# Kernel optimization log

Measured on AMD Instinct MI355X. Metric: run time of the kernel, lower is better.

## Reference

```python
import jax, jax.numpy as jnp
import numpy as np
import math

B, S, D, H, N = 4, 2048, 1024, 8, 128  # batch, seq_len, d_model, n_heads, num_osc
ITERS = 10
DT = 0.1
PI = math.pi


def setup_inputs() -> dict:
    key = jax.random.key(0)
    ks = jax.random.split(key, 5)
    return {
        "x": jax.random.normal(ks[0], (B, S, D), jnp.float32),
        "mask": jnp.ones((B, S), jnp.int32),
        "W_phase": jax.random.normal(ks[1], (D, H * N), jnp.float32) / math.sqrt(D),
        "b_phase": jnp.zeros((H * N,), jnp.float32),
        "natural_freq": jax.random.normal(ks[2], (H, N), jnp.float32) * 0.1,
        "coupling": jnp.ones((H, 1, 1), jnp.float32),  # coupling_strength = 1.0
        "W_out": jax.random.normal(ks[3], (H * N, D), jnp.float32) / math.sqrt(H * N),
        "b_out": jnp.zeros((D,), jnp.float32),
    }


def reference(x, mask, W_phase, b_phase, natural_freq, coupling, W_out, b_out):
    # phases: [B, H, S, N]
    ph = (x @ W_phase + b_phase).reshape(B, S, H, N).transpose(0, 2, 1, 3)
    ph = jnp.tanh(ph) * PI
    m = mask.astype(ph.dtype)[:, None, :, None]  # [B,1,S,1] mask over j
    K = coupling.reshape(1, H, 1, 1)
    w = natural_freq.reshape(1, H, 1, N)

    def step(ph, _):
        s = jnp.sin(ph)
        c = jnp.cos(ph)
        # mean_j m_j * sin(theta_i - theta_j) = sin(th_i)*mean(m*cos) - cos(th_i)*mean(m*sin)
        ms = (m * s).mean(axis=2, keepdims=True)  # [B,H,1,N]
        mc = (m * c).mean(axis=2, keepdims=True)
        dtheta = w + K * (s * mc - c * ms)
        ph2 = jnp.mod(ph + DT * dtheta + PI, 2 * PI) - PI
        return ph2, None

    ph, _ = jax.lax.scan(step, ph, None, length=ITERS)
    # from_phase; dropout is identity in eval mode
    y = ph.transpose(0, 2, 1, 3).reshape(B, S, H * N) @ W_out + b_out
    return y
```

## Files before the change

### kernel.cpp

```cpp
#include <hip/hip_runtime.h>
#include <math.h>

#define S_ 2048
#define D_ 1024
#define HN_ 1024
#define B_ 4
#define M_ 8192
#define K1_ 3072
#define K3_ 1024
#define ITERS_ 10
#define DT_ 0.1f
#define PI_ 3.14159265358979323846f
#define TWOPI_ 6.28318530717958647692f
#define INV2PI_ 0.15915494309189533577f
#define SCALE_ 4096.0f
#define INVSC2_ (1.0f / 16777216.0f)

typedef __attribute__((ext_vector_type(8))) _Float16 f16x8;
typedef __attribute__((ext_vector_type(4))) float f32x4;

__device__ ushort g_xs [(size_t)M_ * K1_];
__device__ ushort g_WpT[(size_t)HN_ * K1_];
__device__ float  g_ph [(size_t)B_ * HN_ * S_];
__device__ ushort g_phh[(size_t)B_ * HN_ * S_];
__device__ ushort g_phT[(size_t)M_ * HN_];
__device__ ushort g_WoT[(size_t)D_ * HN_];

__device__ __forceinline__ ushort f2h(float f) {
    union { _Float16 h; ushort u; } v; v.h = (_Float16)f; return v.u;
}
__device__ __forceinline__ void split2s(float x, ushort& A, ushort& Bc) {
    const float xs = x * SCALE_;
    union { _Float16 h; ushort u; } va, vb;
    va.h = (_Float16)xs;
    const float r = xs - (float)va.h;
    vb.h = (_Float16)r;
    A = va.u; Bc = vb.u;
}
__device__ __forceinline__ void gload16(const void* g, void* l) {
    __builtin_amdgcn_global_load_lds(
        (const __attribute__((address_space(1))) void*)g,
        (__attribute__((address_space(3))) void*)l, 16, 0, 0);
}
__device__ __forceinline__ int pack2(ushort a, ushort b) {
    return (int)(unsigned)a | ((int)(unsigned)b << 16);
}

__global__ __launch_bounds__(256) void split_x(const float* __restrict__ X) {
    const int idx = blockIdx.x * 256 + threadIdx.x;
    const float4 v = ((const float4*)X)[idx];
    const int m  = idx >> 8;
    const int k4 = (idx & 255) * 4;
    ushort a[4], b[4];
    split2s(v.x, a[0], b[0]);
    split2s(v.y, a[1], b[1]);
    split2s(v.z, a[2], b[2]);
    split2s(v.w, a[3], b[3]);
    ushort* row = g_xs + (size_t)m * K1_ + k4;
    int2 oa; oa.x = pack2(a[0], a[1]); oa.y = pack2(a[2], a[3]);
    int2 ob; ob.x = pack2(b[0], b[1]); ob.y = pack2(b[2], b[3]);
    *(int2*)(row)        = oa;
    *(int2*)(row + 1024) = oa;
    *(int2*)(row + 2048) = ob;
}

__global__ __launch_bounds__(256) void splitT_Wp(const float* __restrict__ Wp) {
    __shared__ float t[64][68];
    const int k0 = blockIdx.x * 64;
    const int n0 = blockIdx.y * 64;
    const int r = threadIdx.x >> 2;
    const int c = (threadIdx.x & 3) * 16;
    const float* src = Wp + (size_t)(k0 + r) * HN_ + n0 + c;
    #pragma unroll
    for (int q = 0; q < 4; ++q)
        *(float4*)&t[r][c + 4 * q] = ((const float4*)src)[q];
    __syncthreads();
    ushort ha[16], hb[16];
    #pragma unroll
    for (int j = 0; j < 16; ++j)
        split2s(t[c + j][r], ha[j], hb[j]);
    int4 a0, a1, b0, b1;
    a0.x = pack2(ha[0], ha[1]);   a0.y = pack2(ha[2], ha[3]);
    a0.z = pack2(ha[4], ha[5]);   a0.w = pack2(ha[6], ha[7]);
    a1.x = pack2(ha[8], ha[9]);   a1.y = pack2(ha[10], ha[11]);
    a1.z = pack2(ha[12], ha[13]); a1.w = pack2(ha[14], ha[15]);
    b0.x = pack2(hb[0], hb[1]);   b0.y = pack2(hb[2], hb[3]);
    b0.z = pack2(hb[4], hb[5]);   b0.w = pack2(hb[6], hb[7]);
    b1.x = pack2(hb[8], hb[9]);   b1.y = pack2(hb[10], hb[11]);
    b1.z = pack2(hb[12], hb[13]); b1.w = pack2(hb[14], hb[15]);
    ushort* dst = g_WpT + (size_t)(n0 + r) * K1_ + k0 + c;
    *(int4*)(dst)            = a0; *(int4*)(dst + 8)        = a1;
    *(int4*)(dst + 1024)     = b0; *(int4*)(dst + 1032)     = b1;
    *(int4*)(dst + 2048)     = a0; *(int4*)(dst + 2056)     = a1;
}

__global__ __launch_bounds__(256) void castT_Wo(const float* __restrict__ Wo) {
    __shared__ float t[64][68];
    const int k0 = blockIdx.x * 64;
    const int n0 = blockIdx.y * 64;
    const int r = threadIdx.x >> 2;
    const int c = (threadIdx.x & 3) * 16;
    const float* src = Wo + (size_t)(k0 + r) * D_ + n0 + c;
    #pragma unroll
    for (int q = 0; q < 4; ++q)
        *(float4*)&t[r][c + 4 * q] = ((const float4*)src)[q];
    __syncthreads();
    ushort h[16];
    #pragma unroll
    for (int j = 0; j < 16; ++j) h[j] = f2h(t[c + j][r]);
    ushort* dst = g_WoT + (size_t)(n0 + r) * HN_ + k0 + c;
    int4 o0, o1;
    o0.x = pack2(h[0], h[1]);   o0.y = pack2(h[2], h[3]);
    o0.z = pack2(h[4], h[5]);   o0.w = pack2(h[6], h[7]);
    o1.x = pack2(h[8], h[9]);   o1.y = pack2(h[10], h[11]);
    o1.z = pack2(h[12], h[13]); o1.w = pack2(h[14], h[15]);
    *(int4*)dst = o0;
    *(int4*)(dst + 8) = o1;
}

template<int KDIM>
__device__ __forceinline__ void gemm_mainloop(const ushort* __restrict__ A,
                                              const ushort* __restrict__ Bm,
                                              ushort* lds,
                                              int m0, int n0, int wid, int l,
                                              int wm, int wn,
                                              f32x4 (&acc)[4][4]) {
    constexpr int NT = KDIM / 64;
    const int r8   = l >> 3;
    const int swzo = ((l & 7) * 16) ^ (r8 << 4);

    #define STAGE(T, BUF) do {                                                   \
        const size_t gb_ = (size_t)(T) * 128 + swzo;                             \
        char* ab_ = (char*)lds + (BUF) * 49152;                                  \
        _Pragma("unroll")                                                        \
        for (int j_ = 0; j_ < 4; ++j_) {                                         \
            const int c_ = wid * 4 + j_;                                         \
            gload16((const char*)(A + (size_t)(m0 + c_ * 8 + r8) * KDIM) + gb_,  \
                    ab_ + c_ * 1024);                                            \
        }                                                                        \
        _Pragma("unroll")                                                        \
        for (int j_ = 0; j_ < 2; ++j_) {                                         \
            const int c_ = wid * 2 + j_;                                         \
            gload16((const char*)(Bm + (size_t)(n0 + c_ * 8 + r8) * KDIM) + gb_, \
                    ab_ + 32768 + c_ * 1024);                                    \
        }                                                                        \
    } while (0)

    STAGE(0, 0);
    STAGE(1, 1);

    for (int t = 0; t < NT; ++t) {
        if (t < NT - 1) asm volatile("s_waitcnt vmcnt(6)" ::: "memory");
        else            asm volatile("s_waitcnt vmcnt(0)" ::: "memory");
        __builtin_amdgcn_sched_barrier(0);
        __builtin_amdgcn_s_barrier();
        __builtin_amdgcn_sched_barrier(0);
        if (t + 2 < NT) STAGE(t + 2, (t + 2) % 3);

        const char* ab = (const char*)lds + (t % 3) * 49152;
        const char* bb = ab + 32768;
        #pragma unroll
        for (int ks = 0; ks < 2; ++ks) {
            const int kb = ks * 64 + (l >> 4) * 16;
            f16x8 af[4], bf[4];
            #pragma unroll
            for (int i = 0; i < 4; ++i) {
                const int r = wm * 64 + i * 16 + (l & 15);
                af[i] = *(const f16x8*)(ab + r * 128 + (kb ^ ((r & 7) << 4)));
            }
            #pragma unroll
            for (int i = 0; i < 4; ++i) {
                const int r = wn * 64 + i * 16 + (l & 15);
                bf[i] = *(const f16x8*)(bb + r * 128 + (kb ^ ((r & 7) << 4)));
            }
            __builtin_amdgcn_s_setprio(1);
            #pragma unroll
            for (int i = 0; i < 4; ++i)
                #pragma unroll
                for (int jj = 0; jj < 4; ++jj)
                    acc[i][jj] = __builtin_amdgcn_mfma_f32_16x16x32_f16(af[i], bf[jj], acc[i][jj], 0, 0, 0);
            __builtin_amdgcn_s_setprio(0);
        }
    }
    #undef STAGE
}

__global__ __launch_bounds__(512) void gemm1(const float* __restrict__ bias) {
    __shared__ ushort lds[3 * 24576];
    const int tid = threadIdx.x;
    const int wid = tid >> 6, l = tid & 63;
    const int bid = blockIdx.x;
    const int swz = (bid & 7) * 32 + (bid >> 3);
    const int m0 = (swz & 31) * 256, n0 = (swz >> 5) * 128;
    const int wm = wid >> 1, wn = wid & 1;

    f32x4 acc[4][4];
    #pragma unroll
    for (int i = 0; i < 4; ++i)
        #pragma unroll
        for (int j = 0; j < 4; ++j) acc[i][j] = (f32x4){0.f, 0.f, 0.f, 0.f};

    gemm_mainloop<K1_>(g_xs, g_WpT, lds, m0, n0, wid, l, wm, wn, acc);

    const int r4 = (l >> 4) * 4;
    const int cn = l & 15;
    #pragma unroll
    for (int i = 0; i < 4; ++i) {
        const int mg = m0 + wm * 64 + i * 16 + r4;
        const int bidx = mg >> 11;
        const int sg = mg & 2047;
        #pragma unroll
        for (int jj = 0; jj < 4; ++jj) {
            const int ng = n0 + wn * 64 + jj * 16 + cn;
            const float bb = bias[ng];
            float4 o;
            o.x = PI_ * tanhf(fmaf(acc[i][jj][0], INVSC2_, bb));
            o.y = PI_ * tanhf(fmaf(acc[i][jj][1], INVSC2_, bb));
            o.z = PI_ * tanhf(fmaf(acc[i][jj][2], INVSC2_, bb));
            o.w = PI_ * tanhf(fmaf(acc[i][jj][3], INVSC2_, bb));
            *(float4*)(g_ph + ((size_t)bidx * HN_ + ng) * S_ + sg) = o;
        }
    }
}

__global__ __launch_bounds__(512) void gemm3(const float* __restrict__ bias,
                                             float* __restrict__ Y) {
    __shared__ ushort lds[3 * 24576];
    const int tid = threadIdx.x;
    const int wid = tid >> 6, l = tid & 63;
    const int bid = blockIdx.x;
    const int swz = (bid & 7) * 32 + (bid >> 3);
    const int m0 = (swz & 31) * 256, n0 = (swz >> 5) * 128;
    const int wm = wid >> 1, wn = wid & 1;

    f32x4 acc[4][4];
    #pragma unroll
    for (int i = 0; i < 4; ++i)
        #pragma unroll
        for (int j = 0; j < 4; ++j) acc[i][j] = (f32x4){0.f, 0.f, 0.f, 0.f};

    gemm_mainloop<K3_>(g_phT, g_WoT, lds, m0, n0, wid, l, wm, wn, acc);

    const int r4 = (l >> 4) * 4;
    const int cn = l & 15;
    #pragma unroll
    for (int i = 0; i < 4; ++i) {
        const int mg = m0 + wm * 64 + i * 16 + r4;
        #pragma unroll
        for (int jj = 0; jj < 4; ++jj) {
            const int ng = n0 + wn * 64 + jj * 16 + cn;
            const float bb = bias[ng];
            #pragma unroll
            for (int r = 0; r < 4; ++r)
                Y[(size_t)(mg + r) * D_ + ng] = acc[i][jj][r] + bb;
        }
    }
}

__global__ __launch_bounds__(256) void kuramoto(const int* __restrict__ mask,
                                                const float* __restrict__ natf,
                                                const float* __restrict__ coup) {
    const int wave = blockIdx.x * 4 + (threadIdx.x >> 6);
    const int lane = threadIdx.x & 63;
    const int b = wave >> 10;
    const int hn = wave & 1023;
    const int h = hn >> 7;

    const float wf = natf[hn];
    const float K = coup[h];

    const float* base = g_ph + ((size_t)b * HN_ + hn) * S_;

    float ph[32];
    #pragma unroll
    for (int i = 0; i < 8; ++i) {
        float4 v = *(const float4*)(base + i * 256 + lane * 4);
        ph[4 * i + 0] = v.x; ph[4 * i + 1] = v.y;
        ph[4 * i + 2] = v.z; ph[4 * i + 3] = v.w;
    }

    const int* mb = mask + b * S_;
    unsigned mbits = 0;
    #pragma unroll
    for (int i = 0; i < 8; ++i) {
        int4 mv = *(const int4*)(mb + i * 256 + lane * 4);
        mbits |= (mv.x != 0 ? 1u : 0u) << (4 * i + 0);
        mbits |= (mv.y != 0 ? 1u : 0u) << (4 * i + 1);
        mbits |= (mv.z != 0 ? 1u : 0u) << (4 * i + 2);
        mbits |= (mv.w != 0 ? 1u : 0u) << (4 * i + 3);
    }

    for (int it = 0; it < ITERS_; ++it) {
        float s[32], c[32];
        float ls = 0.f, lc = 0.f;
        #pragma unroll
        for (int i = 0; i < 32; ++i) {
            s[i] = __sinf(ph[i]);
            c[i] = __cosf(ph[i]);
            const float mf = (float)((mbits >> i) & 1u);
            ls = fmaf(mf, s[i], ls);
            lc = fmaf(mf, c[i], lc);
        }
        #pragma unroll
        for (int off = 32; off; off >>= 1) {
            ls += __shfl_xor(ls, off);
            lc += __shfl_xor(lc, off);
        }
        const float ms = ls * (1.f / 2048.f);
        const float mc = lc * (1.f / 2048.f);
        #pragma unroll
        for (int i = 0; i < 32; ++i) {
            const float dth = fmaf(K, fmaf(s[i], mc, -c[i] * ms), wf);
            float t = fmaf(DT_, dth, ph[i]) + PI_;
            t -= TWOPI_ * floorf(t * INV2PI_);
            ph[i] = t - PI_;
        }
    }

    ushort* ob = g_phh + ((size_t)b * HN_ + hn) * S_;
    #pragma unroll
    for (int i = 0; i < 8; ++i) {
        ushort4 o;
        o.x = f2h(ph[4 * i + 0]); o.y = f2h(ph[4 * i + 1]);
        o.z = f2h(ph[4 * i + 2]); o.w = f2h(ph[4 * i + 3]);
        *(ushort4*)(ob + i * 256 + lane * 4) = o;
    }
}

__global__ __launch_bounds__(256) void transpose_ph() {
    __shared__ ushort t[64][72];
    const int b = blockIdx.z;
    const int h0 = blockIdx.y * 64;
    const int s0 = blockIdx.x * 64;
    const int r = threadIdx.x >> 2;
    const int c = (threadIdx.x & 3) * 16;
    const ushort* src = g_phh + ((size_t)b * HN_ + h0 + r) * S_ + s0 + c;
    *(int4*)&t[r][c] = *(const int4*)src;
    *(int4*)&t[r][c + 8] = *(const int4*)(src + 8);
    __syncthreads();
    ushort o[16];
    #pragma unroll
    for (int j = 0; j < 16; ++j) o[j] = t[c + j][r];
    ushort* dst = g_phT + ((size_t)(b * S_ + s0 + r)) * HN_ + h0 + c;
    int4 o0, o1;
    o0.x = pack2(o[0], o[1]);   o0.y = pack2(o[2], o[3]);
    o0.z = pack2(o[4], o[5]);   o0.w = pack2(o[6], o[7]);
    o1.x = pack2(o[8], o[9]);   o1.y = pack2(o[10], o[11]);
    o1.z = pack2(o[12], o[13]); o1.w = pack2(o[14], o[15]);
    *(int4*)dst = o0;
    *(int4*)(dst + 8) = o1;
}

extern "C" void kernel_launch(void* const* d_in, const int* in_sizes, int n_in,
                              void* d_out, int out_size, void* d_ws, size_t ws_size,
                              hipStream_t stream) {
    const float* x    = (const float*)d_in[0];
    const int*   mask = (const int*)d_in[1];
    const float* Wp   = (const float*)d_in[2];
    const float* bp   = (const float*)d_in[3];
    const float* natf = (const float*)d_in[4];
    const float* coup = (const float*)d_in[5];
    const float* Wo   = (const float*)d_in[6];
    const float* bo   = (const float*)d_in[7];
    float* y = (float*)d_out;

    split_x  <<<dim3(8192),         256, 0, stream>>>(x);
    splitT_Wp<<<dim3(16, 16),       256, 0, stream>>>(Wp);
    castT_Wo <<<dim3(16, 16),       256, 0, stream>>>(Wo);
    gemm1    <<<dim3(256),          512, 0, stream>>>(bp);
    kuramoto <<<dim3(1024),         256, 0, stream>>>(mask, natf, coup);
    transpose_ph<<<dim3(32, 16, 4), 256, 0, stream>>>();
    gemm3    <<<dim3(256),          512, 0, stream>>>(bo, y);
}
```

Measured before the change: 174.0 us.

## Split GEMM K-step into two phases interleaving loads with MFMA and remap tiles per XCD

Each 128-wide K tile in the shared GEMM mainloop is now split into two 64-wide halves. Each half reads its LDS fragments, issues half of the next global-to-LDS prefetch (A operand first, then B), barriers, and then runs its MFMAs under raised priority. The aim is to overlap global prefetch issue with matrix math and give finer-grained scheduling. Separately, the block-to-tile mapping is changed so that each XCD gets a contiguous 4x8 patch of output tiles, which should improve L2 reuse of the A and B operands. The trade-off is extra barriers per iteration, and the prefetches now complete on a different schedule relative to the vmcnt(6) wait.

```diff
diff --git a/kernel.cpp b/kernel.cpp
--- a/kernel.cpp
+++ b/kernel.cpp
@@ -129,7 +129,7 @@
     const int r8   = l >> 3;
     const int swzo = ((l & 7) * 16) ^ (r8 << 4);
 
-    #define STAGE(T, BUF) do {                                                   \
+    #define STAGE_A(T, BUF) do {                                                 \
         const size_t gb_ = (size_t)(T) * 128 + swzo;                             \
         char* ab_ = (char*)lds + (BUF) * 49152;                                  \
         _Pragma("unroll")                                                        \
@@ -138,16 +138,20 @@
             gload16((const char*)(A + (size_t)(m0 + c_ * 8 + r8) * KDIM) + gb_,  \
                     ab_ + c_ * 1024);                                            \
         }                                                                        \
+    } while (0)
+    #define STAGE_B(T, BUF) do {                                                 \
+        const size_t gb_ = (size_t)(T) * 128 + swzo;                             \
+        char* bb_ = (char*)lds + (BUF) * 49152 + 32768;                          \
         _Pragma("unroll")                                                        \
         for (int j_ = 0; j_ < 2; ++j_) {                                         \
             const int c_ = wid * 2 + j_;                                         \
             gload16((const char*)(Bm + (size_t)(n0 + c_ * 8 + r8) * KDIM) + gb_, \
-                    ab_ + 32768 + c_ * 1024);                                    \
+                    bb_ + c_ * 1024);                                            \
         }                                                                        \
     } while (0)
 
-    STAGE(0, 0);
-    STAGE(1, 1);
+    STAGE_A(0, 0); STAGE_B(0, 0);
+    STAGE_A(1, 1); STAGE_B(1, 1);
 
     for (int t = 0; t < NT; ++t) {
         if (t < NT - 1) asm volatile("s_waitcnt vmcnt(6)" ::: "memory");
@@ -155,14 +159,14 @@
         __builtin_amdgcn_sched_barrier(0);
         __builtin_amdgcn_s_barrier();
         __builtin_amdgcn_sched_barrier(0);
-        if (t + 2 < NT) STAGE(t + 2, (t + 2) % 3);
 
         const char* ab = (const char*)lds + (t % 3) * 49152;
         const char* bb = ab + 32768;
-        #pragma unroll
-        for (int ks = 0; ks < 2; ++ks) {
-            const int kb = ks * 64 + (l >> 4) * 16;
-            f16x8 af[4], bf[4];
+
+        f16x8 af[4], bf[4];
+
+        {
+            const int kb = (l >> 4) * 16;
             #pragma unroll
             for (int i = 0; i < 4; ++i) {
                 const int r = wm * 64 + i * 16 + (l & 15);
@@ -173,25 +177,65 @@
                 const int r = wn * 64 + i * 16 + (l & 15);
                 bf[i] = *(const f16x8*)(bb + r * 128 + (kb ^ ((r & 7) << 4)));
             }
-            __builtin_amdgcn_s_setprio(1);
-            #pragma unroll
-            for (int i = 0; i < 4; ++i)
-                #pragma unroll
-                for (int jj = 0; jj < 4; ++jj)
-                    acc[i][jj] = __builtin_amdgcn_mfma_f32_16x16x32_f16(af[i], bf[jj], acc[i][jj], 0, 0, 0);
-            __builtin_amdgcn_s_setprio(0);
-        }
-    }
-    #undef STAGE
+        }
+        if (t + 2 < NT) STAGE_A(t + 2, (t + 2) % 3);
+        __builtin_amdgcn_sched_barrier(0);
+        __builtin_amdgcn_s_barrier();
+        asm volatile("s_waitcnt lgkmcnt(0)" ::: "memory");
+        __builtin_amdgcn_sched_barrier(0);
+        __builtin_amdgcn_s_setprio(1);
+        #pragma unroll
+        for (int i = 0; i < 4; ++i)
+            #pragma unroll
+            for (int jj = 0; jj < 4; ++jj)
+                acc[i][jj] = __builtin_amdgcn_mfma_f32_16x16x32_f16(af[i], bf[jj], acc[i][jj], 0, 0, 0);
+        __builtin_amdgcn_s_setprio(0);
+        __builtin_amdgcn_sched_barrier(0);
+
+        {
+            const int kb = 64 + (l >> 4) * 16;
+            #pragma unroll
+            for (int i = 0; i < 4; ++i) {
+                const int r = wm * 64 + i * 16 + (l & 15);
+                af[i] = *(const f16x8*)(ab + r * 128 + (kb ^ ((r & 7) << 4)));
+            }
+            #pragma unroll
+            for (int i = 0; i < 4; ++i) {
+                const int r = wn * 64 + i * 16 + (l & 15);
+                bf[i] = *(const f16x8*)(bb + r * 128 + (kb ^ ((r & 7) << 4)));
+            }
+        }
+        if (t + 2 < NT) STAGE_B(t + 2, (t + 2) % 3);
+        __builtin_amdgcn_sched_barrier(0);
+        __builtin_amdgcn_s_barrier();
+        asm volatile("s_waitcnt lgkmcnt(0)" ::: "memory");
+        __builtin_amdgcn_sched_barrier(0);
+        __builtin_amdgcn_s_setprio(1);
+        #pragma unroll
+        for (int i = 0; i < 4; ++i)
+            #pragma unroll
+            for (int jj = 0; jj < 4; ++jj)
+                acc[i][jj] = __builtin_amdgcn_mfma_f32_16x16x32_f16(af[i], bf[jj], acc[i][jj], 0, 0, 0);
+        __builtin_amdgcn_s_setprio(0);
+        __builtin_amdgcn_sched_barrier(0);
+    }
+    #undef STAGE_A
+    #undef STAGE_B
+}
+
+__device__ __forceinline__ void tile_map(int bid, int& m0, int& n0) {
+    const int xcd = bid & 7;
+    const int idx = bid >> 3;
+    m0 = (xcd * 4 + (idx >> 3)) * 256;
+    n0 = (idx & 7) * 128;
 }
 
 __global__ __launch_bounds__(512) void gemm1(const float* __restrict__ bias) {
     __shared__ ushort lds[3 * 24576];
     const int tid = threadIdx.x;
     const int wid = tid >> 6, l = tid & 63;
-    const int bid = blockIdx.x;
-    const int swz = (bid & 7) * 32 + (bid >> 3);
-    const int m0 = (swz & 31) * 256, n0 = (swz >> 5) * 128;
+    int m0, n0;
+    tile_map(blockIdx.x, m0, n0);
     const int wm = wid >> 1, wn = wid & 1;
 
     f32x4 acc[4][4];
@@ -228,9 +272,8 @@
     __shared__ ushort lds[3 * 24576];
     const int tid = threadIdx.x;
     const int wid = tid >> 6, l = tid & 63;
-    const int bid = blockIdx.x;
-    const int swz = (bid & 7) * 32 + (bid >> 3);
-    const int m0 = (swz & 31) * 256, n0 = (swz >> 5) * 128;
+    int m0, n0;
+    tile_map(blockIdx.x, m0, n0);
     const int wm = wid >> 1, wn = wid & 1;
 
     f32x4 acc[4][4];
```

New measurement: 158.7 us. -8.8%, faster.

## Restructure GEMM mainloop into four interleaved phases with 128x256 tiles

Applied to the files above, without the earlier changes.

Changes the GEMM block tile from 256x128 to 128x256 with a 2x4 wave layout and a new XCD-aware tile mapping. The k-step is split into four phases, each interleaving LDS fragment loads, one slice of the next global stage and a quarter of the MFMAs, separated by barriers. Launch bounds now request two blocks per CU. The aim is to overlap global/LDS traffic with MFMA work and improve L2 locality, at the cost of extra barriers per k-step and more register pressure.

```diff
diff --git a/kernel.cpp b/kernel.cpp
--- a/kernel.cpp
+++ b/kernel.cpp
@@ -128,71 +128,135 @@
     constexpr int NT = KDIM / 64;
     const int r8   = l >> 3;
     const int swzo = ((l & 7) * 16) ^ (r8 << 4);
-
-    #define STAGE(T, BUF) do {                                                   \
-        const size_t gb_ = (size_t)(T) * 128 + swzo;                             \
-        char* ab_ = (char*)lds + (BUF) * 49152;                                  \
-        _Pragma("unroll")                                                        \
-        for (int j_ = 0; j_ < 4; ++j_) {                                         \
-            const int c_ = wid * 4 + j_;                                         \
-            gload16((const char*)(A + (size_t)(m0 + c_ * 8 + r8) * KDIM) + gb_,  \
-                    ab_ + c_ * 1024);                                            \
-        }                                                                        \
-        _Pragma("unroll")                                                        \
-        for (int j_ = 0; j_ < 2; ++j_) {                                         \
-            const int c_ = wid * 2 + j_;                                         \
-            gload16((const char*)(Bm + (size_t)(n0 + c_ * 8 + r8) * KDIM) + gb_, \
-                    ab_ + 32768 + c_ * 1024);                                    \
-        }                                                                        \
-    } while (0)
-
-    STAGE(0, 0);
-    STAGE(1, 1);
-
-    for (int t = 0; t < NT; ++t) {
-        if (t < NT - 1) asm volatile("s_waitcnt vmcnt(6)" ::: "memory");
-        else            asm volatile("s_waitcnt vmcnt(0)" ::: "memory");
-        __builtin_amdgcn_sched_barrier(0);
-        __builtin_amdgcn_s_barrier();
-        __builtin_amdgcn_sched_barrier(0);
-        if (t + 2 < NT) STAGE(t + 2, (t + 2) % 3);
-
-        const char* ab = (const char*)lds + (t % 3) * 49152;
-        const char* bb = ab + 32768;
-        #pragma unroll
-        for (int ks = 0; ks < 2; ++ks) {
-            const int kb = ks * 64 + (l >> 4) * 16;
-            f16x8 af[4], bf[4];
-            #pragma unroll
-            for (int i = 0; i < 4; ++i) {
-                const int r = wm * 64 + i * 16 + (l & 15);
-                af[i] = *(const f16x8*)(ab + r * 128 + (kb ^ ((r & 7) << 4)));
-            }
-            #pragma unroll
-            for (int i = 0; i < 4; ++i) {
-                const int r = wn * 64 + i * 16 + (l & 15);
-                bf[i] = *(const f16x8*)(bb + r * 128 + (kb ^ ((r & 7) << 4)));
-            }
-            __builtin_amdgcn_s_setprio(1);
-            #pragma unroll
-            for (int i = 0; i < 4; ++i)
-                #pragma unroll
-                for (int jj = 0; jj < 4; ++jj)
-                    acc[i][jj] = __builtin_amdgcn_mfma_f32_16x16x32_f16(af[i], bf[jj], acc[i][jj], 0, 0, 0);
-            __builtin_amdgcn_s_setprio(0);
-        }
-    }
-    #undef STAGE
-}
-
-__global__ __launch_bounds__(512) void gemm1(const float* __restrict__ bias) {
+    const int l15  = l & 15;
+    const int kq16 = (l >> 4) * 16;
+
+    #define STG_A(GB, BUF, H)                                                     \
+        gload16((const char*)(A + (size_t)(m0 + (H)*64 + wid*8 + r8) * KDIM) + (GB), \
+                (char*)lds + (BUF)*49152 + ((H)*64 + wid*8)*128)
+    #define STG_B(GB, BUF, H) do {                                                \
+        _Pragma("unroll")                                                         \
+        for (int j_ = 0; j_ < 2; ++j_)                                            \
+            gload16((const char*)(Bm + (size_t)(n0 + (H)*128 + (wid*2+j_)*8 + r8) * KDIM) + (GB), \
+                    (char*)lds + (BUF)*49152 + 16384 + ((H)*128 + (wid*2+j_)*8)*128); \
+    } while (0)
+    #define STG_KT(T, BUF) do {                                                   \
+        const size_t gb_ = (size_t)(T) * 128 + swzo;                              \
+        STG_A(gb_, BUF, 0); STG_A(gb_, BUF, 1);                                   \
+        STG_B(gb_, BUF, 0); STG_B(gb_, BUF, 1);                                   \
+    } while (0)
+
+    #define LD_A(MIB) do {                                                        \
+        _Pragma("unroll")                                                         \
+        for (int mi_ = 0; mi_ < 2; ++mi_)                                         \
+            _Pragma("unroll")                                                     \
+            for (int ks_ = 0; ks_ < 2; ++ks_) {                                   \
+                const int r_ = wm*64 + ((MIB)+mi_)*16 + l15;                      \
+                Aa[mi_][ks_] = *(const f16x8*)(ab + r_*128 +                      \
+                    ((ks_*64 + kq16) ^ ((r_ & 7) << 4)));                         \
+            }                                                                     \
+    } while (0)
+    #define LD_B(NIB) do {                                                        \
+        _Pragma("unroll")                                                         \
+        for (int ni_ = 0; ni_ < 2; ++ni_)                                         \
+            _Pragma("unroll")                                                     \
+            for (int ks_ = 0; ks_ < 2; ++ks_) {                                   \
+                const int r_ = wn*64 + ((NIB)+ni_)*16 + l15;                      \
+                Bb[(NIB)+ni_][ks_] = *(const f16x8*)(bb + r_*128 +                \
+                    ((ks_*64 + kq16) ^ ((r_ & 7) << 4)));                         \
+            }                                                                     \
+    } while (0)
+
+    #define PH_BAR_LGKM do {                                                      \
+        __builtin_amdgcn_sched_barrier(0);                                        \
+        __builtin_amdgcn_s_barrier();                                             \
+        asm volatile("s_waitcnt lgkmcnt(0)" ::: "memory");                        \
+        __builtin_amdgcn_sched_barrier(0);                                        \
+    } while (0)
+    #define PH_BAR do {                                                           \
+        __builtin_amdgcn_sched_barrier(0);                                        \
+        __builtin_amdgcn_s_barrier();                                             \
+        __builtin_amdgcn_sched_barrier(0);                                        \
+    } while (0)
+
+    #define PH_MFMA(MIB, NIB) do {                                                \
+        __builtin_amdgcn_s_setprio(1);                                            \
+        _Pragma("unroll")                                                         \
+        for (int mi_ = 0; mi_ < 2; ++mi_)                                         \
+            _Pragma("unroll")                                                     \
+            for (int ni_ = 0; ni_ < 2; ++ni_)                                     \
+                _Pragma("unroll")                                                 \
+                for (int ks_ = 0; ks_ < 2; ++ks_)                                 \
+                    acc[(MIB)+mi_][(NIB)+ni_] =                                   \
+                        __builtin_amdgcn_mfma_f32_16x16x32_f16(                   \
+                            Aa[mi_][ks_], Bb[(NIB)+ni_][ks_],                     \
+                            acc[(MIB)+mi_][(NIB)+ni_], 0, 0, 0);                  \
+        __builtin_amdgcn_s_setprio(0);                                            \
+        __builtin_amdgcn_sched_barrier(0);                                        \
+    } while (0)
+
+    STG_KT(0, 0);
+    STG_KT(1, 1);
+
+    int bc = 0;
+    for (int kt = 0; kt < NT; ++kt) {
+        if (kt < NT - 1) asm volatile("s_waitcnt vmcnt(6)" ::: "memory");
+        else             asm volatile("s_waitcnt vmcnt(0)" ::: "memory");
+        PH_BAR;
+
+        const char* ab = (const char*)lds + bc * 49152;
+        const char* bb = ab + 16384;
+        int bn = bc + 2; if (bn >= 3) bn -= 3;
+        const bool st = (kt + 2 < NT);
+        const size_t gb = (size_t)(kt + 2) * 128 + swzo;
+
+        f16x8 Aa[2][2], Bb[4][2];
+
+        LD_A(0); LD_B(0);
+        if (st) STG_A(gb, bn, 0);
+        PH_BAR_LGKM;
+        PH_MFMA(0, 0);
+
+        LD_B(2);
+        if (st) STG_A(gb, bn, 1);
+        PH_BAR_LGKM;
+        PH_MFMA(0, 2);
+
+        LD_A(2);
+        if (st) STG_B(gb, bn, 0);
+        PH_BAR_LGKM;
+        PH_MFMA(2, 2);
+
+        if (st) STG_B(gb, bn, 1);
+        PH_BAR;
+        PH_MFMA(2, 0);
+
+        bc = bc + 1; if (bc >= 3) bc -= 3;
+    }
+    #undef STG_A
+    #undef STG_B
+    #undef STG_KT
+    #undef LD_A
+    #undef LD_B
+    #undef PH_BAR_LGKM
+    #undef PH_BAR
+    #undef PH_MFMA
+}
+
+__device__ __forceinline__ void tile_map(int bid, int& m0, int& n0) {
+    const int xcd = bid & 7;
+    const int idx = bid >> 3;
+    m0 = (xcd * 8 + (idx >> 2)) * 128;
+    n0 = (idx & 3) * 256;
+}
+
+__global__ __launch_bounds__(512, 2) void gemm1(const float* __restrict__ bias) {
     __shared__ ushort lds[3 * 24576];
     const int tid = threadIdx.x;
     const int wid = tid >> 6, l = tid & 63;
-    const int bid = blockIdx.x;
-    const int swz = (bid & 7) * 32 + (bid >> 3);
-    const int m0 = (swz & 31) * 256, n0 = (swz >> 5) * 128;
-    const int wm = wid >> 1, wn = wid & 1;
+    int m0, n0;
+    tile_map(blockIdx.x, m0, n0);
+    const int wm = wid >> 2, wn = wid & 3;
 
     f32x4 acc[4][4];
     #pragma unroll
@@ -223,15 +287,14 @@
     }
 }
 
-__global__ __launch_bounds__(512) void gemm3(const float* __restrict__ bias,
-                                             float* __restrict__ Y) {
+__global__ __launch_bounds__(512, 2) void gemm3(const float* __restrict__ bias,
+                                                float* __restrict__ Y) {
     __shared__ ushort lds[3 * 24576];
     const int tid = threadIdx.x;
     const int wid = tid >> 6, l = tid & 63;
-    const int bid = blockIdx.x;
-    const int swz = (bid & 7) * 32 + (bid >> 3);
-    const int m0 = (swz & 31) * 256, n0 = (swz >> 5) * 128;
-    const int wm = wid >> 1, wn = wid & 1;
+    int m0, n0;
+    tile_map(blockIdx.x, m0, n0);
+    const int wm = wid >> 2, wn = wid & 3;
 
     f32x4 acc[4][4];
     #pragma unroll
```

After: 158.6 us. 8.9% less time.

## Shrink GEMM tiles to 128x128 with 4 waves and double-buffered LDS

Applied to the files above, without the earlier changes.

Both GEMMs move from a 256x128 tile with 8 waves and a triple-buffered LDS pipeline to a 128x128 tile with 4 waves and double buffering. This doubles the block count to 512 and adds an XCD-aware tile mapping. LDS fragments are loaded once per stage with precomputed swizzled pointers before the MFMA loop. The aim is better occupancy and load balance across the CUs and less LDS per block. The cost is a shallower prefetch pipeline, an extra barrier per iteration, and lower arithmetic reuse per tile.

```diff
diff --git a/kernel.cpp b/kernel.cpp
--- a/kernel.cpp
+++ b/kernel.cpp
@@ -128,70 +128,86 @@
     constexpr int NT = KDIM / 64;
     const int r8   = l >> 3;
     const int swzo = ((l & 7) * 16) ^ (r8 << 4);
-
-    #define STAGE(T, BUF) do {                                                   \
-        const size_t gb_ = (size_t)(T) * 128 + swzo;                             \
-        char* ab_ = (char*)lds + (BUF) * 49152;                                  \
-        _Pragma("unroll")                                                        \
-        for (int j_ = 0; j_ < 4; ++j_) {                                         \
-            const int c_ = wid * 4 + j_;                                         \
-            gload16((const char*)(A + (size_t)(m0 + c_ * 8 + r8) * KDIM) + gb_,  \
-                    ab_ + c_ * 1024);                                            \
-        }                                                                        \
-        _Pragma("unroll")                                                        \
-        for (int j_ = 0; j_ < 2; ++j_) {                                         \
-            const int c_ = wid * 2 + j_;                                         \
-            gload16((const char*)(Bm + (size_t)(n0 + c_ * 8 + r8) * KDIM) + gb_, \
-                    ab_ + 32768 + c_ * 1024);                                    \
-        }                                                                        \
+    const char* gA = (const char*)(A + (size_t)m0 * KDIM);
+    const char* gB = (const char*)(Bm + (size_t)n0 * KDIM);
+
+    const int thr = (l & 15) * 128;
+    const int f0  = (((l >> 4) * 16)      ^ ((l & 7) << 4));
+    const int f1  = ((64 + (l >> 4) * 16) ^ ((l & 7) << 4));
+    const char* pA0 = (const char*)lds + wm * 8192 + thr + f0;
+    const char* pA1 = (const char*)lds + wm * 8192 + thr + f1;
+    const char* pB0 = (const char*)lds + 16384 + wn * 8192 + thr + f0;
+    const char* pB1 = (const char*)lds + 16384 + wn * 8192 + thr + f1;
+
+    #define STAGE(T, BUF) do {                                                    \
+        const size_t gb_ = (size_t)(T) * 128 + swzo;                              \
+        char* lb_ = (char*)lds + (BUF) * 32768 + wid * 1024;                      \
+        _Pragma("unroll")                                                         \
+        for (int j_ = 0; j_ < 4; ++j_)                                            \
+            gload16(gA + (size_t)(j_ * 32 + wid * 8 + r8) * (KDIM * 2) + gb_,     \
+                    lb_ + j_ * 4096);                                             \
+        _Pragma("unroll")                                                         \
+        for (int j_ = 0; j_ < 4; ++j_)                                            \
+            gload16(gB + (size_t)(j_ * 32 + wid * 8 + r8) * (KDIM * 2) + gb_,     \
+                    lb_ + 16384 + j_ * 4096);                                     \
     } while (0)
 
     STAGE(0, 0);
-    STAGE(1, 1);
-
+
+    #pragma unroll 2
     for (int t = 0; t < NT; ++t) {
-        if (t < NT - 1) asm volatile("s_waitcnt vmcnt(6)" ::: "memory");
-        else            asm volatile("s_waitcnt vmcnt(0)" ::: "memory");
         __builtin_amdgcn_sched_barrier(0);
         __builtin_amdgcn_s_barrier();
         __builtin_amdgcn_sched_barrier(0);
-        if (t + 2 < NT) STAGE(t + 2, (t + 2) % 3);
-
-        const char* ab = (const char*)lds + (t % 3) * 49152;
-        const char* bb = ab + 32768;
-        #pragma unroll
-        for (int ks = 0; ks < 2; ++ks) {
-            const int kb = ks * 64 + (l >> 4) * 16;
-            f16x8 af[4], bf[4];
-            #pragma unroll
-            for (int i = 0; i < 4; ++i) {
-                const int r = wm * 64 + i * 16 + (l & 15);
-                af[i] = *(const f16x8*)(ab + r * 128 + (kb ^ ((r & 7) << 4)));
-            }
-            #pragma unroll
-            for (int i = 0; i < 4; ++i) {
-                const int r = wn * 64 + i * 16 + (l & 15);
-                bf[i] = *(const f16x8*)(bb + r * 128 + (kb ^ ((r & 7) << 4)));
-            }
-            __builtin_amdgcn_s_setprio(1);
+        if (t + 1 < NT) {
+            STAGE(t + 1, (t + 1) & 1);
+            asm volatile("s_waitcnt vmcnt(8)" ::: "memory");
+        } else {
+            asm volatile("s_waitcnt vmcnt(0)" ::: "memory");
+        }
+        __builtin_amdgcn_sched_barrier(0);
+        __builtin_amdgcn_s_barrier();
+        __builtin_amdgcn_sched_barrier(0);
+
+        const int bo = (t & 1) << 15;
+        f16x8 Aa[4][2], Bb[4][2];
+        #pragma unroll
+        for (int i = 0; i < 4; ++i) {
+            Aa[i][0] = *(const f16x8*)(pA0 + bo + i * 2048);
+            Aa[i][1] = *(const f16x8*)(pA1 + bo + i * 2048);
+        }
+        #pragma unroll
+        for (int j = 0; j < 4; ++j) {
+            Bb[j][0] = *(const f16x8*)(pB0 + bo + j * 2048);
+            Bb[j][1] = *(const f16x8*)(pB1 + bo + j * 2048);
+        }
+        __builtin_amdgcn_s_setprio(1);
+        #pragma unroll
+        for (int ks = 0; ks < 2; ++ks)
             #pragma unroll
             for (int i = 0; i < 4; ++i)
                 #pragma unroll
-                for (int jj = 0; jj < 4; ++jj)
-                    acc[i][jj] = __builtin_amdgcn_mfma_f32_16x16x32_f16(af[i], bf[jj], acc[i][jj], 0, 0, 0);
-            __builtin_amdgcn_s_setprio(0);
-        }
+                for (int j = 0; j < 4; ++j)
+                    acc[i][j] = __builtin_amdgcn_mfma_f32_16x16x32_f16(
+                        Aa[i][ks], Bb[j][ks], acc[i][j], 0, 0, 0);
+        __builtin_amdgcn_s_setprio(0);
     }
     #undef STAGE
 }
 
-__global__ __launch_bounds__(512) void gemm1(const float* __restrict__ bias) {
-    __shared__ ushort lds[3 * 24576];
+__device__ __forceinline__ void tile_map(int bid, int& m0, int& n0) {
+    const int xcd = bid & 7;
+    const int idx = bid >> 3;
+    m0 = (xcd * 8 + (idx >> 3)) * 128;
+    n0 = (idx & 7) * 128;
+}
+
+__global__ __launch_bounds__(256) void gemm1(const float* __restrict__ bias) {
+    __shared__ ushort lds[2 * 16384];
     const int tid = threadIdx.x;
     const int wid = tid >> 6, l = tid & 63;
-    const int bid = blockIdx.x;
-    const int swz = (bid & 7) * 32 + (bid >> 3);
-    const int m0 = (swz & 31) * 256, n0 = (swz >> 5) * 128;
+    int m0, n0;
+    tile_map(blockIdx.x, m0, n0);
     const int wm = wid >> 1, wn = wid & 1;
 
     f32x4 acc[4][4];
@@ -223,14 +239,13 @@
     }
 }
 
-__global__ __launch_bounds__(512) void gemm3(const float* __restrict__ bias,
+__global__ __launch_bounds__(256) void gemm3(const float* __restrict__ bias,
                                              float* __restrict__ Y) {
-    __shared__ ushort lds[3 * 24576];
+    __shared__ ushort lds[2 * 16384];
     const int tid = threadIdx.x;
     const int wid = tid >> 6, l = tid & 63;
-    const int bid = blockIdx.x;
-    const int swz = (bid & 7) * 32 + (bid >> 3);
-    const int m0 = (swz & 31) * 256, n0 = (swz >> 5) * 128;
+    int m0, n0;
+    tile_map(blockIdx.x, m0, n0);
     const int wm = wid >> 1, wn = wid & 1;
 
     f32x4 acc[4][4];
@@ -367,8 +382,8 @@
     split_x  <<<dim3(8192),         256, 0, stream>>>(x);
     splitT_Wp<<<dim3(16, 16),       256, 0, stream>>>(Wp);
     castT_Wo <<<dim3(16, 16),       256, 0, stream>>>(Wo);
-    gemm1    <<<dim3(256),          512, 0, stream>>>(bp);
+    gemm1    <<<dim3(512),          256, 0, stream>>>(bp);
     kuramoto <<<dim3(1024),         256, 0, stream>>>(mask, natf, coup);
     transpose_ph<<<dim3(32, 16, 4), 256, 0, stream>>>();
-    gemm3    <<<dim3(256),          512, 0, stream>>>(bo, y);
-}
+    gemm3    <<<dim3(512),          256, 0, stream>>>(bo, y);
+}
```

After: 168.4 us. -3.2%, faster.
